# Kernel tuning notes

Measured on AMD Instinct MI355X. Metric: run time of the kernel, lower is better.

Reference implementation:

```python
import jax, jax.numpy as jnp
import numpy as np

B, T, V, D, H, C = 128, 512, 50000, 128, 256, 10


def _lstm_scan(xs, W, U, b):
    # xs: [T, B, in]; Keras gate order i, f, g(candidate), o.
    xW = jnp.einsum('tbi,ij->tbj', xs, W) + b  # precompute input projection
    Bsz = xs.shape[1]
    Hd = U.shape[0]
    h0 = jnp.zeros((Bsz, Hd), xs.dtype)

    def step(carry, zx):
        h, c = carry
        z = zx + h @ U
        i, f, g, o = jnp.split(z, 4, axis=-1)
        i = jax.nn.sigmoid(i)
        f = jax.nn.sigmoid(f)
        g = jnp.tanh(g)
        o = jax.nn.sigmoid(o)
        c = f * c + i * g
        h = o * jnp.tanh(c)
        return (h, c), h

    (hT, _), hs = jax.lax.scan(step, (h0, h0), xW)
    return hs, hT


def setup_inputs() -> dict:
    key = jax.random.key(0)
    ks = jax.random.split(key, 16)
    f32 = jnp.float32

    def glorot(k, shape):
        fan = shape[0] + shape[1]
        return jax.random.uniform(k, shape, f32, -1.0, 1.0) * np.sqrt(6.0 / fan)

    x = jax.random.randint(ks[0], (B, T), 0, V, dtype=jnp.int32)
    emb = jax.random.normal(ks[1], (V, D), f32) * 0.05
    # layer 1: input D -> 4H per direction
    W1f = glorot(ks[2], (D, 4 * H)); U1f = glorot(ks[3], (H, 4 * H)); b1f = jnp.zeros((4 * H,), f32)
    W1b = glorot(ks[4], (D, 4 * H)); U1b = glorot(ks[5], (H, 4 * H)); b1b = jnp.zeros((4 * H,), f32)
    # layer 2: input 2H -> 4H per direction
    W2f = glorot(ks[6], (2 * H, 4 * H)); U2f = glorot(ks[7], (H, 4 * H)); b2f = jnp.zeros((4 * H,), f32)
    W2b = glorot(ks[8], (2 * H, 4 * H)); U2b = glorot(ks[9], (H, 4 * H)); b2b = jnp.zeros((4 * H,), f32)
    Wd = glorot(ks[10], (2 * H, C)); bd = jnp.zeros((C,), f32)
    return dict(x=x, emb=emb, W1f=W1f, U1f=U1f, b1f=b1f, W1b=W1b, U1b=U1b, b1b=b1b,
                W2f=W2f, U2f=U2f, b2f=b2f, W2b=W2b, U2b=U2b, b2b=b2b, Wd=Wd, bd=bd)


def reference(x, emb, W1f, U1f, b1f, W1b, U1b, b1b, W2f, U2f, b2f, W2b, U2b, b2b, Wd, bd):
    # Embedding lookup -> [T, B, D] (time-major for scan). Dropout is inference-off.
    e = jnp.transpose(emb[x], (1, 0, 2))
    # Bidirectional LSTM 1 (return_sequences)
    hs_f, _ = _lstm_scan(e, W1f, U1f, b1f)
    hs_b, _ = _lstm_scan(e[::-1], W1b, U1b, b1b)
    seq = jnp.concatenate([hs_f, hs_b[::-1]], axis=-1)  # [T, B, 2H]
    # Bidirectional LSTM 2 (return last states)
    _, hT_f = _lstm_scan(seq, W2f, U2f, b2f)
    _, hT_b = _lstm_scan(seq[::-1], W2b, U2b, b2b)
    h = jnp.concatenate([hT_f, hT_b], axis=-1)  # [B, 2H]
    return jax.nn.softmax(h @ Wd + bd, axis=-1)
```

## Files before the change

kernel.cpp:

```cpp
#include <hip/hip_runtime.h>
#include <hip/hip_bf16.h>

#define B_ 128
#define T_ 512
#define H_ 256
#define G4_ 1024
#define D_ 128

typedef short s8v   __attribute__((ext_vector_type(8)));
typedef float f32x4 __attribute__((ext_vector_type(4)));
typedef unsigned short u16x4 __attribute__((ext_vector_type(4)));
typedef unsigned short u16x8 __attribute__((ext_vector_type(8)));
typedef unsigned int   u32x4 __attribute__((ext_vector_type(4)));
typedef unsigned short ush;
typedef unsigned long long ull;

#define BAR_LDS() asm volatile("s_waitcnt lgkmcnt(0)\n\ts_barrier" ::: "memory")

__device__ __forceinline__ void xstore(ull* p, ull v) {
  __hip_atomic_store(p, v, __ATOMIC_RELAXED, __HIP_MEMORY_SCOPE_AGENT);
}
__device__ __forceinline__ ull xload(const ull* p) {
  return __hip_atomic_load(p, __ATOMIC_RELAXED, __HIP_MEMORY_SCOPE_AGENT);
}

__device__ __align__(256) ush   g_xw[(size_t)T_ * 2 * B_ * G4_];
__device__ __align__(256) ush   g_hseq[(size_t)T_ * B_ * 512];
__device__ __align__(256) ull   g_hx2[16 * 2 * 2 * 2 * 512];
__device__ __align__(256) float g_hT[B_ * 512];
__device__ __align__(256) unsigned g_tcnt[512];
__device__ __align__(256) ush   g_wtall[2359296];

__device__ __forceinline__ ush f2b(float f) {
  unsigned u = __builtin_bit_cast(unsigned, f);
  u += 0x7FFFu + ((u >> 16) & 1u);
  return (ush)(u >> 16);
}
__device__ __forceinline__ float b2f(ush h) {
  unsigned u = ((unsigned)h) << 16;
  return __builtin_bit_cast(float, u);
}
__device__ __forceinline__ float sigm(float x) {
  x = fminf(15.f, fmaxf(-15.f, x));
  return 1.f / (1.f + __expf(-x));
}
__device__ __forceinline__ float tanh_(float x) {
  x = fminf(8.f, fmaxf(-8.f, x));
  float e = __expf(-2.f * x);
  return (1.f - e) / (1.f + e);
}

__global__ __launch_bounds__(256, 4) void prep_w(
    const float* __restrict__ Wf, const float* __restrict__ Wb,
    ush* __restrict__ WTf, ush* __restrict__ WTb, int K)
{
  __shared__ ush tile[64][65];
  const float* W = blockIdx.z ? Wb : Wf;
  ush* WT = blockIdx.z ? WTb : WTf;
  int nt = blockIdx.x & 15, kt = blockIdx.x >> 4;
  int tid = threadIdx.x;
  for (int i = tid; i < 4096; i += 256) {
    int k = i >> 6, n = i & 63;
    tile[k][n] = f2b(W[(size_t)(kt * 64 + k) * 1024 + nt * 64 + n]);
  }
  __syncthreads();
  for (int i = tid; i < 4096; i += 256) {
    int n = i >> 6, k = i & 63;
    WT[(size_t)(nt * 64 + n) * K + kt * 64 + k] = tile[k][n];
  }
}

__global__ __launch_bounds__(512, 4) void gemm_xw(
    const int* __restrict__ xi, const float* __restrict__ emb,
    const ush* __restrict__ WTf, const ush* __restrict__ WTb)
{
  __shared__ __align__(16) ush A_lds[128 * 72];
  __shared__ __align__(16) ush BT_lds[128 * 72];
  const int tid = threadIdx.x;
  const int lane = tid & 63;
  const int w = tid >> 6;
  const int nb = blockIdx.x;
  const int t = blockIdx.y;
  const int dir = blockIdx.z;
  const ush* WT = dir ? WTb : WTf;

  const f32x4 zero4 = {0.f, 0.f, 0.f, 0.f};
  f32x4 acc[8];
#pragma unroll
  for (int i = 0; i < 8; ++i) acc[i] = zero4;

  const int rowA0 = tid >> 3;
  const int ccA = tid & 7;
  int idx0 = xi[rowA0 * T_ + t];
  int idx1 = xi[(rowA0 + 64) * T_ + t];

  for (int kc = 0; kc < 2; ++kc) {
    __syncthreads();
    {
      const float* s = emb + (size_t)idx0 * D_ + kc * 64 + ccA * 8;
      f32x4 a = *(const f32x4*)s;
      f32x4 b = *(const f32x4*)(s + 4);
      u16x8 v;
      v[0]=f2b(a[0]); v[1]=f2b(a[1]); v[2]=f2b(a[2]); v[3]=f2b(a[3]);
      v[4]=f2b(b[0]); v[5]=f2b(b[1]); v[6]=f2b(b[2]); v[7]=f2b(b[3]);
      *(u16x8*)&A_lds[rowA0 * 72 + ccA * 8] = v;
    }
    {
      const float* s = emb + (size_t)idx1 * D_ + kc * 64 + ccA * 8;
      f32x4 a = *(const f32x4*)s;
      f32x4 b = *(const f32x4*)(s + 4);
      u16x8 v;
      v[0]=f2b(a[0]); v[1]=f2b(a[1]); v[2]=f2b(a[2]); v[3]=f2b(a[3]);
      v[4]=f2b(b[0]); v[5]=f2b(b[1]); v[6]=f2b(b[2]); v[7]=f2b(b[3]);
      *(u16x8*)&A_lds[(rowA0 + 64) * 72 + ccA * 8] = v;
    }
    {
      int n = tid >> 2, k8 = (tid & 3) * 2;
      const ush* src = WT + (size_t)(nb * 128 + n) * 128 + kc * 64 + k8 * 8;
      *(u32x4*)&BT_lds[n * 72 + k8 * 8] = *(const u32x4*)src;
      *(u32x4*)&BT_lds[n * 72 + k8 * 8 + 8] = *(const u32x4*)(src + 8);
    }
    __syncthreads();
#pragma unroll
    for (int kt = 0; kt < 2; ++kt) {
      const int koff = kt * 32 + ((lane >> 4) << 3);
      s8v af = *(const s8v*)&A_lds[(w * 16 + (lane & 15)) * 72 + koff];
#pragma unroll
      for (int nt = 0; nt < 8; ++nt) {
        s8v bf = *(const s8v*)&BT_lds[(nt * 16 + (lane & 15)) * 72 + koff];
        acc[nt] = __builtin_amdgcn_mfma_f32_16x16x32_bf16(af, bf, acc[nt], 0, 0, 0);
      }
    }
  }
  ush* dst = g_xw + ((size_t)t * 2 + dir) * ((size_t)B_ * G4_);
#pragma unroll
  for (int nt = 0; nt < 8; ++nt) {
    int colg = nb * 128 + nt * 16 + (lane & 15);
    int g = colg >> 8, hc = colg & 255;
#pragma unroll
    for (int jj = 0; jj < 4; ++jj) {
      int row = w * 16 + ((lane >> 4) << 2) + jj;
      dst[(size_t)row * 1024 + hc * 4 + g] = f2b(acc[nt][jj]);
    }
  }
}

__global__ __launch_bounds__(512, 2) void mega(
    int layer, const ush* __restrict__ UTf, const ush* __restrict__ UTb,
    const float* __restrict__ bfp, const float* __restrict__ bbp,
    int writeSeq, int ngemm,
    const ush* __restrict__ WT2f, const ush* __restrict__ WT2b)
{
  __shared__ __align__(16) ush smem[2 * 128 * 72];
  const int bx = blockIdx.x;
  const int tid = threadIdx.x;
  const int lane = tid & 63;
  const int w = tid >> 6;
  const int l15 = lane & 15;
  const int lq = lane >> 4;

  if (bx < 64) {
    const int slice = bx & 15;
    const int dir = (bx >> 4) & 1;
    const int nh = bx >> 5;
    const ush* UT = dir ? UTb : UTf;
    const float* bias = dir ? bbp : bfp;
    const int mycol = nh * 128 + w * 16 + l15;
    const int rowb = slice * 8;
    const unsigned sbase = (unsigned)(layer * T_);
    ush* h0 = smem;

    s8v bfrO[4][4], bfrP[4][4];
#pragma unroll
    for (int g = 0; g < 4; ++g) {
      const ush* up = UT + (size_t)(g * 256 + mycol) * 256;
#pragma unroll
      for (int i = 0; i < 4; ++i) {
        bfrO[g][i] = *(const s8v*)(up + (nh * 128 + i * 32) + lq * 8);
        bfrP[g][i] = *(const s8v*)(up + ((nh ^ 1) * 128 + i * 32) + lq * 8);
      }
    }
    float bias_r[4];
#pragma unroll
    for (int g = 0; g < 4; ++g) bias_r[g] = bias[g * 256 + mycol];

    {
      ull* z = (ull*)smem;
      z[tid] = 0ull; z[tid + 512] = 0ull; z[tid + 1024] = 0ull; z[tid + 1536] = 0ull;
    }
    __syncthreads();

    float c_[4] = {0.f, 0.f, 0.f, 0.f};
    ull* hx_sd = g_hx2 + (size_t)(slice * 2 + dir) * 2048;

    const int w_src = tid >> 6, r_ = tid & 63;
    const int blkc = r_ >> 5, lqs = (r_ >> 4) & 1, l15s = r_ & 15;
    const int col_p = (nh ^ 1) * 128 + w_src * 16 + l15s;
    const int r0c = lqs * 4 + blkc * 2;
    const int c8p = col_p >> 3, wp = col_p & 7;
    const int sw0 = ((c8p ^ r0c) & 31) * 8 + wp;
    const int sw1 = ((c8p ^ (r0c + 1)) & 31) * 8 + wp;
    const int xrow = (lq & 1) * 4;

    u16x4 xv[4];
    {
      int t0 = dir ? (T_ - 1) : 0;
      const ush* xp = g_xw + (((size_t)t0 * 2 + dir) * B_ + rowb) * 1024 + mycol * 4;
#pragma unroll
      for (int j = 0; j < 4; ++j) xv[j] = *(const u16x4*)(xp + (size_t)(xrow + j) * 1024);
    }

    const f32x4 zero4 = {0.f, 0.f, 0.f, 0.f};
    f32x4 acc[4];
#pragma unroll
    for (int g = 0; g < 4; ++g) acc[g] = zero4;

    for (int s = 0; s < T_; ++s) {
      const int p = s & 1;
      if (s > 0) {
        const ull* ap = hx_sd + (size_t)(p * 2 + (nh ^ 1)) * 512 + tid;
        unsigned target = sbase + (unsigned)s;
        ull v;
        for (;;) {
          v = xload(ap);
          if ((unsigned)(v >> 32) >= target) break;
          __builtin_amdgcn_s_sleep(1);
        }
        ush* dl = h0 + p * 4096;
        dl[r0c * 256 + sw0] = (ush)v;
        dl[(r0c + 1) * 256 + sw1] = (ush)(v >> 16);
      }
      BAR_LDS();
      if (writeSeq) {
        if (tid == 0 && s >= 2) {
          int td = dir ? (T_ + 1 - s) : (s - 2);
          __hip_atomic_fetch_add(&g_tcnt[td], 1u, __ATOMIC_RELAXED, __HIP_MEMORY_SCOPE_AGENT);
        }
        if (s > 0 && tid < 128) {
          int row8 = tid >> 4, idx = tid & 15;
          int col = nh * 128 + idx * 8;
          int c8 = col >> 3;
          const ush* srcl = h0 + p * 4096 + row8 * 256 + ((c8 ^ row8) & 31) * 8;
          ull lo = *(const ull*)srcl;
          ull hi = *(const ull*)(srcl + 4);
          int tprev = dir ? (T_ - s) : (s - 1);
          ull* dst = (ull*)&g_hseq[((size_t)tprev * B_ + rowb + row8) * 512 + dir * 256 + col];
          xstore(dst, lo);
          xstore(dst + 1, hi);
        }
      }
      {
        s8v afP[4];
#pragma unroll
        for (int i = 0; i < 4; ++i) {
          int c8 = ((nh ^ 1) * 4 + i) * 4 + lq;
          afP[i] = *(const s8v*)(h0 + p * 4096 + l15 * 256 + ((c8 ^ l15) & 31) * 8);
        }
#pragma unroll
        for (int i = 0; i < 4; ++i) {
#pragma unroll
          for (int g = 0; g < 4; ++g)
            acc[g] = __builtin_amdgcn_mfma_f32_16x16x32_bf16(afP[i], bfrP[g][i], acc[g], 0, 0, 0);
        }
      }
      ush hv[4];
#pragma unroll
      for (int j = 0; j < 4; ++j) {
        float vi = acc[0][j] + b2f(xv[j][0]) + bias_r[0];
        float vf = acc[1][j] + b2f(xv[j][1]) + bias_r[1];
        float vg = acc[2][j] + b2f(xv[j][2]) + bias_r[2];
        float vo = acc[3][j] + b2f(xv[j][3]) + bias_r[3];
        float ig = sigm(vi), fg = sigm(vf), gg = tanh_(vg), og = sigm(vo);
        float cc = fg * c_[j] + ig * gg;
        c_[j] = cc;
        hv[j] = f2b(og * tanh_(cc));
      }
      u16x4 xn[4];
      {
        int tn = dir ? max(0, T_ - 2 - s) : min(T_ - 1, s + 1);
        const ush* xp = g_xw + (((size_t)tn * 2 + dir) * B_ + rowb) * 1024 + mycol * 4;
#pragma unroll
        for (int j = 0; j < 4; ++j) xn[j] = *(const u16x4*)(xp + (size_t)(xrow + j) * 1024);
      }
      if (lq < 2 && s + 1 < T_) {
        ull seqw = ((ull)(sbase + (unsigned)s + 1u)) << 32;
        ull e0 = (ull)hv[0] | ((ull)hv[1] << 16) | seqw;
        ull e1 = (ull)hv[2] | ((ull)hv[3] << 16) | seqw;
        ull* ep = hx_sd + (size_t)((p ^ 1) * 2 + nh) * 512 + w * 64 + lq * 16 + l15;
        xstore(ep, e0);
        xstore(ep + 32, e1);
      }
      if (lq < 2) {
        int c8o = mycol >> 3, wo = mycol & 7;
        ush* dl = h0 + (p ^ 1) * 4096;
#pragma unroll
        for (int j = 0; j < 4; ++j) {
          int r = lq * 4 + j;
          dl[r * 256 + (((c8o ^ r) & 31) * 8 + wo)] = hv[j];
        }
      }
      BAR_LDS();
#pragma unroll
      for (int g = 0; g < 4; ++g) acc[g] = zero4;
      {
        s8v afO[4];
#pragma unroll
        for (int i = 0; i < 4; ++i) {
          int c8 = (nh * 4 + i) * 4 + lq;
          afO[i] = *(const s8v*)(h0 + (p ^ 1) * 4096 + l15 * 256 + ((c8 ^ l15) & 31) * 8);
        }
#pragma unroll
        for (int i = 0; i < 4; ++i) {
#pragma unroll
          for (int g = 0; g < 4; ++g)
            acc[g] = __builtin_amdgcn_mfma_f32_16x16x32_bf16(afO[i], bfrO[g][i], acc[g], 0, 0, 0);
        }
      }
#pragma unroll
      for (int j = 0; j < 4; ++j) xv[j] = xn[j];
    }
    __syncthreads();
    const ush* bufl = h0 + (T_ & 1) * 4096;
    if (writeSeq) {
      if (tid < 128) {
        int row8 = tid >> 4, idx = tid & 15;
        int col = nh * 128 + idx * 8;
        int c8 = col >> 3;
        const ush* srcl = bufl + row8 * 256 + ((c8 ^ row8) & 31) * 8;
        ull lo = *(const ull*)srcl;
        ull hi = *(const ull*)(srcl + 4);
        int tlast = dir ? 0 : (T_ - 1);
        ull* dst = (ull*)&g_hseq[((size_t)tlast * B_ + rowb + row8) * 512 + dir * 256 + col];
        xstore(dst, lo);
        xstore(dst + 1, hi);
      }
      asm volatile("s_waitcnt vmcnt(0)" ::: "memory");
      __syncthreads();
      if (tid == 0) {
        int ta = dir ? 1 : (T_ - 2);
        int tb2 = dir ? 0 : (T_ - 1);
        __hip_atomic_fetch_add(&g_tcnt[ta], 1u, __ATOMIC_RELAXED, __HIP_MEMORY_SCOPE_AGENT);
        __hip_atomic_fetch_add(&g_tcnt[tb2], 1u, __ATOMIC_RELAXED, __HIP_MEMORY_SCOPE_AGENT);
      }
    } else {
      if (tid < 128) {
        int row8 = tid >> 4, idx = tid & 15;
        int col = nh * 128 + idx * 8;
        int c8 = col >> 3;
        const ush* srcl = bufl + row8 * 256 + ((c8 ^ row8) & 31) * 8;
        float* dstf = g_hT + (size_t)(rowb + row8) * 512 + dir * 256 + col;
        f32x4 f0, f1;
#pragma unroll
        for (int j = 0; j < 4; ++j) { f0[j] = b2f(srcl[j]); f1[j] = b2f(srcl[4 + j]); }
        *(f32x4*)dstf = f0;
        *(f32x4*)(dstf + 4) = f1;
      }
    }
  } else {
    if (ngemm <= 0) return;
    ush* A_lds = smem;
    ush* BT_lds = smem + 128 * 72;
    const int wg = bx - 64;
    const int rowA0 = tid >> 3;
    const int ccA = tid & 7;

    for (int u = wg; u < 8192; u += ngemm) {
      int pairIdx = u >> 4, sub = u & 15;
      int nb = sub & 7, gdir = sub >> 3;
      int t = (pairIdx & 1) ? (255 - (pairIdx >> 1)) : (256 + (pairIdx >> 1));
      const ush* WT = gdir ? WT2b : WT2f;
      for (;;) {
        unsigned v = __hip_atomic_load(&g_tcnt[t], __ATOMIC_RELAXED, __HIP_MEMORY_SCOPE_AGENT);
        if (v >= 64u) break;
        __builtin_amdgcn_s_sleep(4);
      }
      const f32x4 zero4 = {0.f, 0.f, 0.f, 0.f};
      f32x4 acc[8];
#pragma unroll
      for (int i = 0; i < 8; ++i) acc[i] = zero4;
      for (int kc = 0; kc < 8; ++kc) {
        __syncthreads();
        {
          const ush* s0 = g_hseq + ((size_t)(t * B_ + rowA0)) * 512 + kc * 64 + ccA * 8;
          *(u32x4*)&A_lds[rowA0 * 72 + ccA * 8] = *(const u32x4*)s0;
          const ush* s1 = g_hseq + ((size_t)(t * B_ + rowA0 + 64)) * 512 + kc * 64 + ccA * 8;
          *(u32x4*)&A_lds[(rowA0 + 64) * 72 + ccA * 8] = *(const u32x4*)s1;
        }
        {
          int n = tid >> 2, k8 = (tid & 3) * 2;
          const ush* src = WT + (size_t)(nb * 128 + n) * 512 + kc * 64 + k8 * 8;
          *(u32x4*)&BT_lds[n * 72 + k8 * 8] = *(const u32x4*)src;
          *(u32x4*)&BT_lds[n * 72 + k8 * 8 + 8] = *(const u32x4*)(src + 8);
        }
        __syncthreads();
#pragma unroll
        for (int kt = 0; kt < 2; ++kt) {
          const int koff = kt * 32 + (lq << 3);
          s8v af = *(const s8v*)&A_lds[(w * 16 + l15) * 72 + koff];
#pragma unroll
          for (int nt = 0; nt < 8; ++nt) {
            s8v bf = *(const s8v*)&BT_lds[(nt * 16 + l15) * 72 + koff];
            acc[nt] = __builtin_amdgcn_mfma_f32_16x16x32_bf16(af, bf, acc[nt], 0, 0, 0);
          }
        }
      }
      ush* dst = g_xw + ((size_t)t * 2 + gdir) * ((size_t)B_ * G4_);
#pragma unroll
      for (int nt = 0; nt < 8; ++nt) {
        int colg = nb * 128 + nt * 16 + l15;
        int g = colg >> 8, hc = colg & 255;
#pragma unroll
        for (int jj = 0; jj < 4; ++jj) {
          int row = w * 16 + (lq << 2) + jj;
          dst[(size_t)row * 1024 + hc * 4 + g] = f2b(acc[nt][jj]);
        }
      }
    }
  }
}

__global__ __launch_bounds__(512, 1) void dense_softmax(
    const float* __restrict__ Wd, const float* __restrict__ bd, float* __restrict__ out)
{
  __shared__ float wT[10 * 512];
  __shared__ float part[512 * 10];
  int tid = threadIdx.x;
  for (int i = tid; i < 5120; i += 512) {
    int k = i / 10, j = i - k * 10;
    wT[j * 512 + k] = Wd[i];
  }
  __syncthreads();
  int row = tid >> 2, q = tid & 3;
  float acc[10];
#pragma unroll
  for (int j = 0; j < 10; ++j) acc[j] = 0.f;
  const float* hrow = g_hT + (size_t)row * 512 + q * 128;
  for (int kk = 0; kk < 32; ++kk) {
    f32x4 h4 = *(const f32x4*)(hrow + kk * 4);
#pragma unroll
    for (int j = 0; j < 10; ++j) {
      f32x4 w4 = *(const f32x4*)&wT[j * 512 + q * 128 + kk * 4];
      acc[j] += h4[0] * w4[0] + h4[1] * w4[1] + h4[2] * w4[2] + h4[3] * w4[3];
    }
  }
#pragma unroll
  for (int j = 0; j < 10; ++j) part[tid * 10 + j] = acc[j];
  __syncthreads();
  if (tid < 128) {
    float lg[10];
#pragma unroll
    for (int j = 0; j < 10; ++j)
      lg[j] = bd[j] + part[(tid * 4 + 0) * 10 + j] + part[(tid * 4 + 1) * 10 + j]
                    + part[(tid * 4 + 2) * 10 + j] + part[(tid * 4 + 3) * 10 + j];
    float m = lg[0];
#pragma unroll
    for (int j = 1; j < 10; ++j) m = fmaxf(m, lg[j]);
    float ssum = 0.f;
#pragma unroll
    for (int j = 0; j < 10; ++j) { lg[j] = __expf(lg[j] - m); ssum += lg[j]; }
    float inv = 1.f / ssum;
#pragma unroll
    for (int j = 0; j < 10; ++j) out[tid * 10 + j] = lg[j] * inv;
  }
}

extern "C" void kernel_launch(void* const* d_in, const int* in_sizes, int n_in,
                              void* d_out, int out_size, void* d_ws, size_t ws_size,
                              hipStream_t stream) {
  (void)in_sizes; (void)n_in; (void)d_ws; (void)ws_size; (void)out_size;
  const int* x = (const int*)d_in[0];
  const float* emb = (const float*)d_in[1];
  const float* W1f = (const float*)d_in[2];
  const float* U1f = (const float*)d_in[3];
  const float* b1f = (const float*)d_in[4];
  const float* W1b = (const float*)d_in[5];
  const float* U1b = (const float*)d_in[6];
  const float* b1b = (const float*)d_in[7];
  const float* W2f = (const float*)d_in[8];
  const float* U2f = (const float*)d_in[9];
  const float* b2f = (const float*)d_in[10];
  const float* W2b = (const float*)d_in[11];
  const float* U2b = (const float*)d_in[12];
  const float* b2b = (const float*)d_in[13];
  const float* Wd  = (const float*)d_in[14];
  const float* bd  = (const float*)d_in[15];
  float* out = (float*)d_out;

  void* hx_p = nullptr; void* wt_p = nullptr; void* tc_p = nullptr;
  hipGetSymbolAddress(&hx_p, HIP_SYMBOL(g_hx2));
  hipGetSymbolAddress(&wt_p, HIP_SYMBOL(g_wtall));
  hipGetSymbolAddress(&tc_p, HIP_SYMBOL(g_tcnt));
  ush* wt = (ush*)wt_p;
  hipMemsetAsync(hx_p, 0, sizeof(ull) * 16 * 2 * 2 * 2 * 512, stream);
  hipMemsetAsync(tc_p, 0, sizeof(unsigned) * 512, stream);

  ush* wt1f = wt;                 ush* wt1b = wt1f + 131072;
  ush* ut1f = wt1b + 131072;      ush* ut1b = ut1f + 262144;
  ush* wt2f = ut1b + 262144;      ush* wt2b = wt2f + 524288;
  ush* ut2f = wt2b + 524288;      ush* ut2b = ut2f + 262144;

  prep_w<<<dim3(32, 1, 2), 256, 0, stream>>>(W1f, W1b, wt1f, wt1b, 128);
  prep_w<<<dim3(64, 1, 2), 256, 0, stream>>>(U1f, U1b, ut1f, ut1b, 256);
  prep_w<<<dim3(128, 1, 2), 256, 0, stream>>>(W2f, W2b, wt2f, wt2b, 512);
  prep_w<<<dim3(64, 1, 2), 256, 0, stream>>>(U2f, U2b, ut2f, ut2b, 256);

  gemm_xw<<<dim3(8, T_, 2), 512, 0, stream>>>(x, emb, wt1f, wt1b);
  mega<<<256, 512, 0, stream>>>(0, ut1f, ut1b, b1f, b1b, 1, 192, wt2f, wt2b);
  mega<<<64, 512, 0, stream>>>(1, ut2f, ut2b, b2f, b2b, 0, 0, nullptr, nullptr);
  dense_softmax<<<1, 512, 0, stream>>>(Wd, bd, out);
}
```

Measured before the change: 3.267 ms.

## Add dedicated export wavefront to LSTM recurrence blocks for global exchange

Each recurrence block gets a ninth wavefront that handles the cross-block hidden-state exchange writes, the hidden-sequence stores and the timestep counter increments. The eight compute wavefronts now only do the MFMA and gate math and write h into LDS. The export wave reads h back from LDS after the barrier and publishes it with sequence tags. The aim is to take global stores and atomics off the compute waves' critical path, at the cost of an extra LDS read and a longer chain between computing h and publishing it. Block size grows to 576, and the GEMM branch gates its work with tid<512.

```diff
diff --git a/kernel.cpp b/kernel.cpp
--- a/kernel.cpp
+++ b/kernel.cpp
@@ -145,7 +145,7 @@
   }
 }
 
-__global__ __launch_bounds__(512, 2) void mega(
+__global__ __launch_bounds__(576, 2) void mega(
     int layer, const ush* __restrict__ UTf, const ush* __restrict__ UTb,
     const float* __restrict__ bfp, const float* __restrict__ bbp,
     int writeSeq, int ngemm,
@@ -165,28 +165,32 @@
     const int nh = bx >> 5;
     const ush* UT = dir ? UTb : UTf;
     const float* bias = dir ? bbp : bfp;
-    const int mycol = nh * 128 + w * 16 + l15;
+    const bool isComp = (w < 8);
+    const bool isExp = (w == 8);
+    const int mycol = nh * 128 + (w & 7) * 16 + l15;
     const int rowb = slice * 8;
     const unsigned sbase = (unsigned)(layer * T_);
     ush* h0 = smem;
 
     s8v bfrO[4][4], bfrP[4][4];
-#pragma unroll
-    for (int g = 0; g < 4; ++g) {
-      const ush* up = UT + (size_t)(g * 256 + mycol) * 256;
-#pragma unroll
-      for (int i = 0; i < 4; ++i) {
-        bfrO[g][i] = *(const s8v*)(up + (nh * 128 + i * 32) + lq * 8);
-        bfrP[g][i] = *(const s8v*)(up + ((nh ^ 1) * 128 + i * 32) + lq * 8);
-      }
-    }
     float bias_r[4];
-#pragma unroll
-    for (int g = 0; g < 4; ++g) bias_r[g] = bias[g * 256 + mycol];
+    if (isComp) {
+#pragma unroll
+      for (int g = 0; g < 4; ++g) {
+        const ush* up = UT + (size_t)(g * 256 + mycol) * 256;
+#pragma unroll
+        for (int i = 0; i < 4; ++i) {
+          bfrO[g][i] = *(const s8v*)(up + (nh * 128 + i * 32) + lq * 8);
+          bfrP[g][i] = *(const s8v*)(up + ((nh ^ 1) * 128 + i * 32) + lq * 8);
+        }
+      }
+#pragma unroll
+      for (int g = 0; g < 4; ++g) bias_r[g] = bias[g * 256 + mycol];
+    }
 
     {
       ull* z = (ull*)smem;
-      z[tid] = 0ull; z[tid + 512] = 0ull; z[tid + 1024] = 0ull; z[tid + 1536] = 0ull;
+      for (int i = tid; i < 2048; i += 576) z[i] = 0ull;
     }
     __syncthreads();
 
@@ -201,9 +205,10 @@
     const int sw0 = ((c8p ^ r0c) & 31) * 8 + wp;
     const int sw1 = ((c8p ^ (r0c + 1)) & 31) * 8 + wp;
     const int xrow = (lq & 1) * 4;
+    const int rbE = ((lane >> 4) & 1) * 4 + ((lane >> 5) & 1) * 2;
 
     u16x4 xv[4];
-    {
+    if (isComp) {
       int t0 = dir ? (T_ - 1) : 0;
       const ush* xp = g_xw + (((size_t)t0 * 2 + dir) * B_ + rowb) * 1024 + mycol * 4;
 #pragma unroll
@@ -217,7 +222,7 @@
 
     for (int s = 0; s < T_; ++s) {
       const int p = s & 1;
-      if (s > 0) {
+      if (s > 0 && tid < 512) {
         const ull* ap = hx_sd + (size_t)(p * 2 + (nh ^ 1)) * 512 + tid;
         unsigned target = sbase + (unsigned)s;
         ull v;
@@ -231,78 +236,92 @@
         dl[(r0c + 1) * 256 + sw1] = (ush)(v >> 16);
       }
       BAR_LDS();
-      if (writeSeq) {
-        if (tid == 0 && s >= 2) {
+      if (isExp && writeSeq) {
+        asm volatile("s_waitcnt vmcnt(0)" ::: "memory");
+        if (lane == 0 && s >= 2) {
           int td = dir ? (T_ + 1 - s) : (s - 2);
           __hip_atomic_fetch_add(&g_tcnt[td], 1u, __ATOMIC_RELAXED, __HIP_MEMORY_SCOPE_AGENT);
         }
-        if (s > 0 && tid < 128) {
-          int row8 = tid >> 4, idx = tid & 15;
-          int col = nh * 128 + idx * 8;
-          int c8 = col >> 3;
-          const ush* srcl = h0 + p * 4096 + row8 * 256 + ((c8 ^ row8) & 31) * 8;
-          ull lo = *(const ull*)srcl;
-          ull hi = *(const ull*)(srcl + 4);
-          int tprev = dir ? (T_ - s) : (s - 1);
-          ull* dst = (ull*)&g_hseq[((size_t)tprev * B_ + rowb + row8) * 512 + dir * 256 + col];
-          xstore(dst, lo);
-          xstore(dst + 1, hi);
-        }
-      }
-      {
-        s8v afP[4];
-#pragma unroll
-        for (int i = 0; i < 4; ++i) {
-          int c8 = ((nh ^ 1) * 4 + i) * 4 + lq;
-          afP[i] = *(const s8v*)(h0 + p * 4096 + l15 * 256 + ((c8 ^ l15) & 31) * 8);
-        }
-#pragma unroll
-        for (int i = 0; i < 4; ++i) {
-#pragma unroll
-          for (int g = 0; g < 4; ++g)
-            acc[g] = __builtin_amdgcn_mfma_f32_16x16x32_bf16(afP[i], bfrP[g][i], acc[g], 0, 0, 0);
-        }
-      }
-      ush hv[4];
-#pragma unroll
-      for (int j = 0; j < 4; ++j) {
-        float vi = acc[0][j] + b2f(xv[j][0]) + bias_r[0];
-        float vf = acc[1][j] + b2f(xv[j][1]) + bias_r[1];
-        float vg = acc[2][j] + b2f(xv[j][2]) + bias_r[2];
-        float vo = acc[3][j] + b2f(xv[j][3]) + bias_r[3];
-        float ig = sigm(vi), fg = sigm(vf), gg = tanh_(vg), og = sigm(vo);
-        float cc = fg * c_[j] + ig * gg;
-        c_[j] = cc;
-        hv[j] = f2b(og * tanh_(cc));
-      }
-      u16x4 xn[4];
-      {
-        int tn = dir ? max(0, T_ - 2 - s) : min(T_ - 1, s + 1);
-        const ush* xp = g_xw + (((size_t)tn * 2 + dir) * B_ + rowb) * 1024 + mycol * 4;
-#pragma unroll
-        for (int j = 0; j < 4; ++j) xn[j] = *(const u16x4*)(xp + (size_t)(xrow + j) * 1024);
-      }
-      if (lq < 2 && s + 1 < T_) {
+        if (s > 0) {
+#pragma unroll
+          for (int it = 0; it < 2; ++it) {
+            int row8 = (lane >> 4) + it * 4;
+            int col = nh * 128 + (lane & 15) * 8;
+            int c8 = col >> 3;
+            const ush* srcl = h0 + p * 4096 + row8 * 256 + ((c8 ^ row8) & 31) * 8;
+            ull lo = *(const ull*)srcl;
+            ull hi = *(const ull*)(srcl + 4);
+            int tprev = dir ? (T_ - s) : (s - 1);
+            ull* dst = (ull*)&g_hseq[((size_t)tprev * B_ + rowb + row8) * 512 + dir * 256 + col];
+            xstore(dst, lo);
+            xstore(dst + 1, hi);
+          }
+        }
+      }
+      if (isComp) {
+        u16x4 xn[4];
+        {
+          int tn = dir ? max(0, T_ - 2 - s) : min(T_ - 1, s + 1);
+          const ush* xp = g_xw + (((size_t)tn * 2 + dir) * B_ + rowb) * 1024 + mycol * 4;
+#pragma unroll
+          for (int j = 0; j < 4; ++j) xn[j] = *(const u16x4*)(xp + (size_t)(xrow + j) * 1024);
+        }
+        {
+          s8v afP[4];
+#pragma unroll
+          for (int i = 0; i < 4; ++i) {
+            int c8 = ((nh ^ 1) * 4 + i) * 4 + lq;
+            afP[i] = *(const s8v*)(h0 + p * 4096 + l15 * 256 + ((c8 ^ l15) & 31) * 8);
+          }
+#pragma unroll
+          for (int i = 0; i < 4; ++i) {
+#pragma unroll
+            for (int g = 0; g < 4; ++g)
+              acc[g] = __builtin_amdgcn_mfma_f32_16x16x32_bf16(afP[i], bfrP[g][i], acc[g], 0, 0, 0);
+          }
+        }
+        ush hv[4];
+#pragma unroll
+        for (int j = 0; j < 4; ++j) {
+          float vi = acc[0][j] + b2f(xv[j][0]) + bias_r[0];
+          float vf = acc[1][j] + b2f(xv[j][1]) + bias_r[1];
+          float vg = acc[2][j] + b2f(xv[j][2]) + bias_r[2];
+          float vo = acc[3][j] + b2f(xv[j][3]) + bias_r[3];
+          float ig = sigm(vi), fg = sigm(vf), gg = tanh_(vg), og = sigm(vo);
+          float cc = fg * c_[j] + ig * gg;
+          c_[j] = cc;
+          hv[j] = f2b(og * tanh_(cc));
+        }
+        if (lq < 2) {
+          int c8o = mycol >> 3, wo = mycol & 7;
+          ush* dl = h0 + (p ^ 1) * 4096;
+#pragma unroll
+          for (int j = 0; j < 4; ++j) {
+            int r = lq * 4 + j;
+            dl[r * 256 + (((c8o ^ r) & 31) * 8 + wo)] = hv[j];
+          }
+        }
+#pragma unroll
+        for (int j = 0; j < 4; ++j) xv[j] = xn[j];
+      }
+      BAR_LDS();
+      if (isExp) {
         ull seqw = ((ull)(sbase + (unsigned)s + 1u)) << 32;
-        ull e0 = (ull)hv[0] | ((ull)hv[1] << 16) | seqw;
-        ull e1 = (ull)hv[2] | ((ull)hv[3] << 16) | seqw;
-        ull* ep = hx_sd + (size_t)((p ^ 1) * 2 + nh) * 512 + w * 64 + lq * 16 + l15;
-        xstore(ep, e0);
-        xstore(ep + 32, e1);
-      }
-      if (lq < 2) {
-        int c8o = mycol >> 3, wo = mycol & 7;
-        ush* dl = h0 + (p ^ 1) * 4096;
-#pragma unroll
-        for (int j = 0; j < 4; ++j) {
-          int r = lq * 4 + j;
-          dl[r * 256 + (((c8o ^ r) & 31) * 8 + wo)] = hv[j];
-        }
-      }
-      BAR_LDS();
-#pragma unroll
-      for (int g = 0; g < 4; ++g) acc[g] = zero4;
-      {
+        const ush* bufn = h0 + (p ^ 1) * 4096;
+        ull* eb = hx_sd + (size_t)((p ^ 1) * 2 + nh) * 512;
+#pragma unroll
+        for (int j = 0; j < 8; ++j) {
+          int col = nh * 128 + j * 16 + l15;
+          int c8 = col >> 3, wo = col & 7;
+          ush v0 = bufn[rbE * 256 + (((c8 ^ rbE) & 31) * 8 + wo)];
+          ush v1 = bufn[(rbE + 1) * 256 + (((c8 ^ (rbE + 1)) & 31) * 8 + wo)];
+          ull e = (ull)v0 | ((ull)v1 << 16) | seqw;
+          xstore(eb + j * 64 + lane, e);
+        }
+      }
+      if (isComp) {
+#pragma unroll
+        for (int g = 0; g < 4; ++g) acc[g] = zero4;
         s8v afO[4];
 #pragma unroll
         for (int i = 0; i < 4; ++i) {
@@ -316,8 +335,6 @@
             acc[g] = __builtin_amdgcn_mfma_f32_16x16x32_bf16(afO[i], bfrO[g][i], acc[g], 0, 0, 0);
         }
       }
-#pragma unroll
-      for (int j = 0; j < 4; ++j) xv[j] = xn[j];
     }
     __syncthreads();
     const ush* bufl = h0 + (T_ & 1) * 4096;
@@ -380,39 +397,41 @@
       for (int i = 0; i < 8; ++i) acc[i] = zero4;
       for (int kc = 0; kc < 8; ++kc) {
         __syncthreads();
-        {
+        if (tid < 512) {
           const ush* s0 = g_hseq + ((size_t)(t * B_ + rowA0)) * 512 + kc * 64 + ccA * 8;
           *(u32x4*)&A_lds[rowA0 * 72 + ccA * 8] = *(const u32x4*)s0;
           const ush* s1 = g_hseq + ((size_t)(t * B_ + rowA0 + 64)) * 512 + kc * 64 + ccA * 8;
           *(u32x4*)&A_lds[(rowA0 + 64) * 72 + ccA * 8] = *(const u32x4*)s1;
-        }
-        {
           int n = tid >> 2, k8 = (tid & 3) * 2;
           const ush* src = WT + (size_t)(nb * 128 + n) * 512 + kc * 64 + k8 * 8;
           *(u32x4*)&BT_lds[n * 72 + k8 * 8] = *(const u32x4*)src;
           *(u32x4*)&BT_lds[n * 72 + k8 * 8 + 8] = *(const u32x4*)(src + 8);
         }
         __syncthreads();
-#pragma unroll
-        for (int kt = 0; kt < 2; ++kt) {
-          const int koff = kt * 32 + (lq << 3);
-          s8v af = *(const s8v*)&A_lds[(w * 16 + l15) * 72 + koff];
-#pragma unroll
-          for (int nt = 0; nt < 8; ++nt) {
-            s8v bf = *(const s8v*)&BT_lds[(nt * 16 + l15) * 72 + koff];
-            acc[nt] = __builtin_amdgcn_mfma_f32_16x16x32_bf16(af, bf, acc[nt], 0, 0, 0);
+        if (tid < 512) {
+#pragma unroll
+          for (int kt = 0; kt < 2; ++kt) {
+            const int koff = kt * 32 + (lq << 3);
+            s8v af = *(const s8v*)&A_lds[((w & 7) * 16 + l15) * 72 + koff];
+#pragma unroll
+            for (int nt = 0; nt < 8; ++nt) {
+              s8v bf = *(const s8v*)&BT_lds[(nt * 16 + l15) * 72 + koff];
+              acc[nt] = __builtin_amdgcn_mfma_f32_16x16x32_bf16(af, bf, acc[nt], 0, 0, 0);
+            }
           }
         }
       }
-      ush* dst = g_xw + ((size_t)t * 2 + gdir) * ((size_t)B_ * G4_);
-#pragma unroll
-      for (int nt = 0; nt < 8; ++nt) {
-        int colg = nb * 128 + nt * 16 + l15;
-        int g = colg >> 8, hc = colg & 255;
-#pragma unroll
-        for (int jj = 0; jj < 4; ++jj) {
-          int row = w * 16 + (lq << 2) + jj;
-          dst[(size_t)row * 1024 + hc * 4 + g] = f2b(acc[nt][jj]);
+      if (tid < 512) {
+        ush* dst = g_xw + ((size_t)t * 2 + gdir) * ((size_t)B_ * G4_);
+#pragma unroll
+        for (int nt = 0; nt < 8; ++nt) {
+          int colg = nb * 128 + nt * 16 + l15;
+          int g = colg >> 8, hc = colg & 255;
+#pragma unroll
+          for (int jj = 0; jj < 4; ++jj) {
+            int row = (w & 7) * 16 + (lq << 2) + jj;
+            dst[(size_t)row * 1024 + hc * 4 + g] = f2b(acc[nt][jj]);
+          }
         }
       }
     }
@@ -505,7 +524,7 @@
   prep_w<<<dim3(64, 1, 2), 256, 0, stream>>>(U2f, U2b, ut2f, ut2b, 256);
 
   gemm_xw<<<dim3(8, T_, 2), 512, 0, stream>>>(x, emb, wt1f, wt1b);
-  mega<<<256, 512, 0, stream>>>(0, ut1f, ut1b, b1f, b1b, 1, 192, wt2f, wt2b);
-  mega<<<64, 512, 0, stream>>>(1, ut2f, ut2b, b2f, b2b, 0, 0, nullptr, nullptr);
+  mega<<<256, 576, 0, stream>>>(0, ut1f, ut1b, b1f, b1b, 1, 192, wt2f, wt2b);
+  mega<<<64, 576, 0, stream>>>(1, ut2f, ut2b, b2f, b2b, 0, 0, nullptr, nullptr);
   dense_softmax<<<1, 512, 0, stream>>>(Wd, bd, out);
 }
```

After: 8.060 ms. +146.7%, slower.
